# Kernel optimization log

Hardware: AMD Instinct MI355X
Metric: run time of the kernel (lower is better)

Reference implementation:

```python
import jax, jax.numpy as jnp
import numpy as np

NUM_FEATURE = 128  # bins; linear in_features = NUM_FEATURE + 1
VECTOR_DIM = 64


def setup_inputs() -> dict:
    key = jax.random.key(0)
    k1, k2, k3 = jax.random.split(key, 3)
    x = jax.random.randint(k1, (8192, 200), 0, NUM_FEATURE + 1)
    # nn.Linear(num_feature+1, vector_dim): W is (out, in) = (64, 129)
    W = jax.random.normal(k2, (VECTOR_DIM, NUM_FEATURE + 1), dtype=jnp.float32) * 0.05
    b = jax.random.normal(k3, (VECTOR_DIM,), dtype=jnp.float32) * 0.05
    return {"x": x, "W": W, "b": b}


def reference(x, W, b):
    # embeddings = tril(ones)[x] has ones in columns 0..x (inclusive), so
    # embeddings @ W.T = sum_{j<=x} W[:, j] = cumsum(W, axis=1)[:, x].
    # This avoids materializing the (..., F+1) one-hot-prefix tensor.
    Wc = jnp.cumsum(W, axis=1)              # (D, F+1)
    out = jnp.take(Wc.T, x, axis=0) + b     # (8192, 200, D)
    return out
```

## Files before the change

### kernel.cpp

```cpp
#include <hip/hip_runtime.h>


constexpr int F1     = 129;
constexpr int D      = 64;
constexpr int ROWS   = 8192 * 200;
constexpr int TOTAL4 = ROWS * D / 4;
constexpr int TBL_F  = F1 * D;
constexpr int TBL4   = TBL_F / 4;

constexpr int BLOCKS = 1024;
constexpr int TPB    = 256;
constexpr int ITERS  = TOTAL4 / (BLOCKS * TPB);

typedef float floatx4 __attribute__((ext_vector_type(4)));

__global__ void build_table_kernel(const float* __restrict__ W,
                                   const float* __restrict__ b,
                                   float* __restrict__ tbl) {
    int d = threadIdx.x;
    if (d >= D) return;
    float bias = b[d];
    float acc = 0.0f;
    for (int j = 0; j < F1; ++j) {
        acc += W[d * F1 + j];
        tbl[j * D + d] = acc + bias;
    }
}

__global__ __launch_bounds__(TPB) void embed_main_kernel(
        const int* __restrict__ x,
        const float* __restrict__ tbl,
        float* __restrict__ out) {
    __shared__ floatx4 lds_tbl[TBL4];
    const floatx4* t4 = (const floatx4*)tbl;
    for (int i = threadIdx.x; i < TBL4; i += TPB)
        lds_tbl[i] = t4[i];
    __syncthreads();

    floatx4* out4 = (floatx4*)out;
    const int base = blockIdx.x * TPB + threadIdx.x;
#pragma unroll 4
    for (int it = 0; it < ITERS; ++it) {
        int gid  = it * (BLOCKS * TPB) + base;
        int row  = gid >> 4;
        int quad = gid & 15;
        int xi   = x[row];
        floatx4 v = lds_tbl[xi * 16 + quad];
        __builtin_nontemporal_store(v, &out4[gid]);
    }
}

extern "C" void kernel_launch(void* const* d_in, const int* in_sizes, int n_in,
                              void* d_out, int out_size, void* d_ws, size_t ws_size,
                              hipStream_t stream) {
    const int*   x = (const int*)  d_in[0];
    const float* W = (const float*)d_in[1];
    const float* b = (const float*)d_in[2];
    float* out = (float*)d_out;
    float* tbl = (float*)d_ws;

    build_table_kernel<<<1, 64, 0, stream>>>(W, b, tbl);
    embed_main_kernel<<<BLOCKS, TPB, 0, stream>>>(x, tbl, out);
}
```

Before: 443.9 us.

## Give each block a contiguous row range with x staged in LDS

The main kernel now assigns each block a contiguous chunk of rows and preloads that chunk's indices into shared memory, so the per-element global x loads become LDS reads. Output stores switch from nontemporal to regular stores and become contiguous per block instead of grid-strided. The table-build kernel now stages W in LDS with a 256-thread block to make the cumsum's reads cheaper. The cost is extra LDS per block (about 6.4 KB for indices) and a possible change in cache behaviour for the large output write.

```diff
diff --git a/kernel.cpp b/kernel.cpp
--- a/kernel.cpp
+++ b/kernel.cpp
@@ -1,29 +1,35 @@
 #include <hip/hip_runtime.h>
 
 
-constexpr int F1     = 129;
-constexpr int D      = 64;
-constexpr int ROWS   = 8192 * 200;
-constexpr int TOTAL4 = ROWS * D / 4;
-constexpr int TBL_F  = F1 * D;
-constexpr int TBL4   = TBL_F / 4;
+constexpr int F1   = 129;
+constexpr int D    = 64;
+constexpr int ROWS = 8192 * 200;
+constexpr int TBL_F = F1 * D;
+constexpr int TBL4  = TBL_F / 4;
 
 constexpr int BLOCKS = 1024;
 constexpr int TPB    = 256;
-constexpr int ITERS  = TOTAL4 / (BLOCKS * TPB);
+constexpr int ROWS_PER_BLOCK = ROWS / BLOCKS;
+constexpr int Q_PER_BLOCK    = ROWS_PER_BLOCK * D / 4;
+constexpr int ITERS          = Q_PER_BLOCK / TPB;
 
 typedef float floatx4 __attribute__((ext_vector_type(4)));
 
-__global__ void build_table_kernel(const float* __restrict__ W,
-                                   const float* __restrict__ b,
-                                   float* __restrict__ tbl) {
+__global__ __launch_bounds__(TPB) void build_table_kernel(
+        const float* __restrict__ W,
+        const float* __restrict__ b,
+        float* __restrict__ tbl) {
+    __shared__ float ldsW[TBL_F];
+    for (int i = threadIdx.x; i < TBL_F; i += TPB)
+        ldsW[i] = W[i];
+    __syncthreads();
     int d = threadIdx.x;
-    if (d >= D) return;
-    float bias = b[d];
-    float acc = 0.0f;
-    for (int j = 0; j < F1; ++j) {
-        acc += W[d * F1 + j];
-        tbl[j * D + d] = acc + bias;
+    if (d < D) {
+        float acc = b[d];
+        for (int j = 0; j < F1; ++j) {
+            acc += ldsW[d * F1 + j];
+            tbl[j * D + d] = acc;
+        }
     }
 }
 
@@ -32,21 +38,23 @@
         const float* __restrict__ tbl,
         float* __restrict__ out) {
     __shared__ floatx4 lds_tbl[TBL4];
+    __shared__ int     lds_x[ROWS_PER_BLOCK];
+
     const floatx4* t4 = (const floatx4*)tbl;
     for (int i = threadIdx.x; i < TBL4; i += TPB)
         lds_tbl[i] = t4[i];
+    const int row0 = blockIdx.x * ROWS_PER_BLOCK;
+    for (int i = threadIdx.x; i < ROWS_PER_BLOCK; i += TPB)
+        lds_x[i] = x[row0 + i];
     __syncthreads();
 
-    floatx4* out4 = (floatx4*)out;
-    const int base = blockIdx.x * TPB + threadIdx.x;
+    floatx4* out4 = (floatx4*)out + (size_t)blockIdx.x * Q_PER_BLOCK;
 #pragma unroll 4
     for (int it = 0; it < ITERS; ++it) {
-        int gid  = it * (BLOCKS * TPB) + base;
-        int row  = gid >> 4;
-        int quad = gid & 15;
-        int xi   = x[row];
-        floatx4 v = lds_tbl[xi * 16 + quad];
-        __builtin_nontemporal_store(v, &out4[gid]);
+        int j    = it * TPB + threadIdx.x;
+        int xi   = lds_x[j >> 4];
+        floatx4 v = lds_tbl[xi * 16 + (j & 15)];
+        out4[j] = v;
     }
 }
 
@@ -59,6 +67,6 @@
     float* out = (float*)d_out;
     float* tbl = (float*)d_ws;
 
-    build_table_kernel<<<1, 64, 0, stream>>>(W, b, tbl);
+    build_table_kernel<<<1, TPB, 0, stream>>>(W, b, tbl);
     embed_main_kernel<<<BLOCKS, TPB, 0, stream>>>(x, tbl, out);
 }
```

Result: faster. 427.8 us (-3.6%).
